# Kernel optimization log

Hardware: AMD Instinct MI355X
Metric: run time of the kernel (lower is better)

Reference implementation:

```python
import jax, jax.numpy as jnp
import numpy as np

G = 251            # grid_size = int(1e6 ** 0.4)
ORDER = 3          # KAN_SPLINE_ORDER
NB = G + ORDER     # num_basis = 254
H = (1.05 - (-0.05)) / G
# grid: [-order .. G+order] * h + lo  -> length G + 2*ORDER + 1 = 258 (same for every feature)
GRID = jnp.arange(-ORDER, G + ORDER + 1, dtype=jnp.float32) * H + (-0.05)
EPS = 1e-8


def bsplines(x):
    # x: [B, in] -> bases: [B, in, NB] via Cox-de Boor recursion
    x = x[..., None]
    b = ((x >= GRID[:-1]) & (x < GRID[1:])).astype(x.dtype)
    for k in range(1, ORDER + 1):
        left = (x - GRID[:-(k + 1)]) / jnp.maximum(GRID[k:-1] - GRID[:-(k + 1)], EPS)
        right = (GRID[k + 1:] - x) / jnp.maximum(GRID[k + 1:] - GRID[1:-k], EPS)
        b = left * b[..., :-1] + right * b[..., 1:]
    return b


def kan_layer(x, bw, sw, wb, ws, residual):
    # base path: SiLU then linear
    base = jax.nn.silu(x) @ bw.T                      # [B, out]
    # spline path: basis [B, in*NB] @ spline_weight.reshape(out, in*NB).T
    bas = bsplines(x).reshape(x.shape[0], -1)
    spl = bas @ sw.reshape(sw.shape[0], -1).T         # [B, out]
    out = wb * base + ws * spl
    return out + x if residual else out


def setup_inputs() -> dict:
    key = jax.random.key(0)
    ks = jax.random.split(key, 20)
    B, D, W = 2048, 64, 256
    d = {"x": jax.random.uniform(ks[0], (B, D), dtype=jnp.float32)}
    dims = [(W, D), (W, W), (W, W), (1, W)]
    for i, (o, inp) in enumerate(dims):
        d[f"bw{i}"] = jax.random.normal(ks[1 + 4 * i], (o, inp), dtype=jnp.float32) * 0.05
        d[f"sw{i}"] = jax.random.normal(ks[2 + 4 * i], (o, inp, NB), dtype=jnp.float32) * (0.5 / G)
        d[f"wb{i}"] = jnp.ones((1,), jnp.float32)
        d[f"ws{i}"] = jnp.ones((1,), jnp.float32)
    return d


def reference(x, bw0, sw0, wb0, ws0, bw1, sw1, wb1, ws1, bw2, sw2, wb2, ws2, bw3, sw3, wb3, ws3):
    h = kan_layer(x, bw0, sw0, wb0, ws0, False)   # input layer, no residual (64 -> 256)
    h = kan_layer(h, bw1, sw1, wb1, ws1, True)    # hidden, residual (256 -> 256)
    h = kan_layer(h, bw2, sw2, wb2, ws2, True)    # hidden, residual (256 -> 256)
    return kan_layer(h, bw3, sw3, wb3, ws3, False)  # output layer (256 -> 1)
```

## Files before the change

kernel.cpp:

```cpp
#include <hip/hip_runtime.h>

#define BATCH 2048
#define NB 254

typedef float f4u __attribute__((ext_vector_type(4), aligned(4)));

__device__ __forceinline__ float selw(int pd, float w0, float w1, float w2, float w3) {
    return (pd == 0) ? w0 : (pd == 1) ? w1 : (pd == 2) ? w2 : (pd == 3) ? w3 : 0.f;
}

template<bool TR>
__global__ __launch_bounds__(256) void basis_kernel(
    const float* __restrict__ act, int IN,
    const float* __restrict__ wbp, const float* __restrict__ wsp,
    float2* __restrict__ sjbuf, float4* __restrict__ vbuf)
{
    int idx = blockIdx.x * 256 + threadIdx.x;
    int total = BATCH * IN;
    if (idx >= total) return;
    int i = idx / BATCH;
    int b = idx - i * BATCH;

    float x = TR ? act[idx] : act[(size_t)b * IN + i];
    float wb = wbp[0], wsc = wsp[0];

    float sil = x / (1.f + __expf(-x));

    const float LO = -0.05f;
    const float INVH = 228.18181818181818f;
    float uf = (x - LO) * INVH;
    float fm = floorf(uf);
    float t = uf - fm;
    int M = (int)fm + 3;

    bool valid = (M >= 0) && (M <= 256);
    float wsv = valid ? wsc : 0.f;

    float omt = 1.f - t;
    float t2 = t * t, t3 = t2 * t;
    const float S = 1.f / 6.f;
    float w0 = omt * omt * omt * S * wsv;
    float w1 = (3.f * t3 - 6.f * t2 + 4.f) * S * wsv;
    float w2 = (-3.f * t3 + 3.f * t2 + 3.f * t + 1.f) * S * wsv;
    float w3 = t3 * S * wsv;

    int js = M - 3;
    js = js < 0 ? 0 : js;
    js = js > (NB - 4) ? (NB - 4) : js;
    if (!valid) js = 0;
    int d = js - (M - 3);

    float vp0 = selw(0 + d, w0, w1, w2, w3);
    float vp1 = selw(1 + d, w0, w1, w2, w3);
    float vp2 = selw(2 + d, w0, w1, w2, w3);
    float vp3 = selw(3 + d, w0, w1, w2, w3);

    sjbuf[idx] = make_float2(sil * wb, __int_as_float(js));
    vbuf[idx] = make_float4(vp0, vp1, vp2, vp3);
}

template<int IN, int OT, bool RES, int IG, int BT>
__global__ __launch_bounds__(BT * IG) void accum_f32(
    const float2* __restrict__ sjbuf, const float4* __restrict__ vbuf,
    const float* __restrict__ bw, const float* __restrict__ sw,
    const float* __restrict__ resid, float* __restrict__ out)
{
    int bx = threadIdx.x;
    int g  = threadIdx.y;
    int b  = blockIdx.y * BT + bx;
    int o0 = blockIdx.x * OT;

    float acc[OT];
#pragma unroll
    for (int k = 0; k < OT; k++) acc[k] = 0.f;

    const size_t ostride = (size_t)IN * NB;
    const int CH = IN / IG;
    const int i0 = g * CH;

    for (int ii = 0; ii < CH; ii++) {
        int i = i0 + ii;
        float2 sj = sjbuf[i * BATCH + b];
        float4 v = vbuf[i * BATCH + b];
        int j = __float_as_int(sj.y);
        float s = sj.x;
        const float* p = sw + (size_t)(o0 * IN + i) * NB + j;
        const float* bq = bw + (size_t)o0 * IN + i;

        f4u w[OT];
#pragma unroll
        for (int oo = 0; oo < OT; oo++)
            w[oo] = *(const f4u*)(p + (size_t)oo * ostride);

#pragma unroll
        for (int oo = 0; oo < OT; oo++) {
            float bwv = bq[oo * IN];
            acc[oo] += s * bwv + v.x * w[oo][0] + v.y * w[oo][1] + v.z * w[oo][2] + v.w * w[oo][3];
        }
    }

    __shared__ float lds[OT * (IG - 1) * BT];
    if (g > 0) {
#pragma unroll
        for (int oo = 0; oo < OT; oo++)
            lds[(oo * (IG - 1) + (g - 1)) * BT + bx] = acc[oo];
    }
    __syncthreads();
    if (g == 0) {
#pragma unroll
        for (int oo = 0; oo < OT; oo++) {
            float a = acc[oo];
            for (int gg = 1; gg < IG; gg++)
                a += lds[(oo * (IG - 1) + (gg - 1)) * BT + bx];
            size_t oidx = (size_t)(o0 + oo) * BATCH + b;
            float r = RES ? resid[oidx] : 0.f;
            out[oidx] = a + r;
        }
    }
}

__global__ __launch_bounds__(256) void out_kernel(
    const float2* __restrict__ sjbuf, const float4* __restrict__ vbuf,
    const float* __restrict__ bw, const float* __restrict__ sw,
    float* __restrict__ out)
{
    int tid = threadIdx.x;
    int bl = tid >> 6;
    int ig = tid & 63;
    int b = blockIdx.x * 4 + bl;

    float acc = 0.f;
    for (int ii = ig; ii < 256; ii += 64) {
        float2 sj = sjbuf[ii * BATCH + b];
        float4 v = vbuf[ii * BATCH + b];
        int j = __float_as_int(sj.y);
        const float* p = sw + (size_t)ii * NB + j;
        acc += sj.x * bw[ii] + v.x * p[0] + v.y * p[1] + v.z * p[2] + v.w * p[3];
    }
#pragma unroll
    for (int dlt = 32; dlt >= 1; dlt >>= 1) acc += __shfl_down(acc, dlt, 64);
    if (ig == 0) out[b] = acc;
}

extern "C" void kernel_launch(void* const* d_in, const int* in_sizes, int n_in,
                              void* d_out, int out_size, void* d_ws, size_t ws_size,
                              hipStream_t stream)
{
    const float* x   = (const float*)d_in[0];
    const float* bw0 = (const float*)d_in[1];
    const float* sw0 = (const float*)d_in[2];
    const float* wb0 = (const float*)d_in[3];
    const float* ws0 = (const float*)d_in[4];
    const float* bw1 = (const float*)d_in[5];
    const float* sw1 = (const float*)d_in[6];
    const float* wb1 = (const float*)d_in[7];
    const float* ws1 = (const float*)d_in[8];
    const float* bw2 = (const float*)d_in[9];
    const float* sw2 = (const float*)d_in[10];
    const float* wb2 = (const float*)d_in[11];
    const float* ws2 = (const float*)d_in[12];
    const float* bw3 = (const float*)d_in[13];
    const float* sw3 = (const float*)d_in[14];
    const float* wb3 = (const float*)d_in[15];
    const float* ws3 = (const float*)d_in[16];

    char* ws = (char*)d_ws;
    float4* vbuf  = (float4*)(ws);
    float2* sjbuf = (float2*)(ws + 8  * 1024 * 1024);
    float*  hA    = (float*)(ws + 12 * 1024 * 1024);
    float*  hB    = (float*)(ws + 14 * 1024 * 1024);

    float* out = (float*)d_out;

    dim3 ablk(64, 8);
    dim3 agrd(32, 32);

    basis_kernel<false><<<(BATCH * 64 + 255) / 256, 256, 0, stream>>>(x, 64, wb0, ws0, sjbuf, vbuf);
    accum_f32<64, 8, false, 8, 64><<<agrd, ablk, 0, stream>>>(sjbuf, vbuf, bw0, sw0, nullptr, hA);

    basis_kernel<true><<<(BATCH * 256 + 255) / 256, 256, 0, stream>>>(hA, 256, wb1, ws1, sjbuf, vbuf);
    accum_f32<256, 8, true, 8, 64><<<agrd, ablk, 0, stream>>>(sjbuf, vbuf, bw1, sw1, hA, hB);

    basis_kernel<true><<<(BATCH * 256 + 255) / 256, 256, 0, stream>>>(hB, 256, wb2, ws2, sjbuf, vbuf);
    accum_f32<256, 8, true, 8, 64><<<agrd, ablk, 0, stream>>>(sjbuf, vbuf, bw2, sw2, hB, hA);

    basis_kernel<true><<<(BATCH * 256 + 255) / 256, 256, 0, stream>>>(hA, 256, wb3, ws3, sjbuf, vbuf);
    out_kernel<<<BATCH / 4, 256, 0, stream>>>(sjbuf, vbuf, bw3, sw3, out);
}
```

Baseline: 295.2 us.

## Transpose spline weights to basis-major layout and use batch-major accumulation

```diff
diff --git a/kernel.cpp b/kernel.cpp
--- a/kernel.cpp
+++ b/kernel.cpp
@@ -9,7 +9,7 @@
     return (pd == 0) ? w0 : (pd == 1) ? w1 : (pd == 2) ? w2 : (pd == 3) ? w3 : 0.f;
 }
 
-template<bool TR>
+template<bool TR, bool BI>
 __global__ __launch_bounds__(256) void basis_kernel(
     const float* __restrict__ act, int IN,
     const float* __restrict__ wbp, const float* __restrict__ wsp,
@@ -18,10 +18,11 @@
     int idx = blockIdx.x * 256 + threadIdx.x;
     int total = BATCH * IN;
     if (idx >= total) return;
-    int i = idx / BATCH;
-    int b = idx - i * BATCH;
-
-    float x = TR ? act[idx] : act[(size_t)b * IN + i];
+    int i, b;
+    if (BI) { b = idx / IN; i = idx - b * IN; }
+    else    { i = idx / BATCH; b = idx - i * BATCH; }
+
+    float x = TR ? act[i * BATCH + b] : act[(size_t)b * IN + i];
     float wb = wbp[0], wsc = wsp[0];
 
     float sil = x / (1.f + __expf(-x));
@@ -57,6 +58,98 @@
 
     sjbuf[idx] = make_float2(sil * wb, __int_as_float(js));
     vbuf[idx] = make_float4(vp0, vp1, vp2, vp3);
+}
+
+__global__ __launch_bounds__(256) void transpose_sw(
+    const float* __restrict__ src, float* __restrict__ dst, int IN)
+{
+    __shared__ float lds[64][68];
+    int i  = blockIdx.z;
+    int c0 = blockIdx.y * 64;
+    int o0 = blockIdx.x * 64;
+    int t  = threadIdx.x;
+    int q16 = (t & 15) * 4;
+    int row = t >> 4;
+
+    for (int r = 0; r < 4; r++) {
+        int o = row + r * 16;
+        int c = c0 + q16;
+        const float* sp = src + ((size_t)(o0 + o) * IN + i) * NB + c;
+        if (c + 3 < NB) {
+            f4u v = *(const f4u*)sp;
+            lds[o][q16 + 0] = v[0]; lds[o][q16 + 1] = v[1];
+            lds[o][q16 + 2] = v[2]; lds[o][q16 + 3] = v[3];
+        } else {
+            for (int q = 0; q < 4; q++)
+                lds[o][q16 + q] = (c + q < NB) ? sp[q] : 0.f;
+        }
+    }
+    __syncthreads();
+    for (int r = 0; r < 4; r++) {
+        int cl = row + r * 16;
+        int c = c0 + cl;
+        if (c < NB) {
+            float4 v = make_float4(lds[q16 + 0][cl], lds[q16 + 1][cl],
+                                   lds[q16 + 2][cl], lds[q16 + 3][cl]);
+            *(float4*)(dst + ((size_t)i * NB + c) * 256 + o0 + q16) = v;
+        }
+    }
+}
+
+__global__ __launch_bounds__(256) void transpose_bw(
+    const float* __restrict__ src, float* __restrict__ dst, int IN, int O)
+{
+    __shared__ float lds[64][65];
+    int o0 = blockIdx.x * 64, i0 = blockIdx.y * 64;
+    int t = threadIdx.x; int tx = t & 63, ty = t >> 6;
+    for (int r = 0; r < 16; r++) {
+        int o = ty + r * 4;
+        lds[o][tx] = src[(size_t)(o0 + o) * IN + i0 + tx];
+    }
+    __syncthreads();
+    for (int r = 0; r < 16; r++) {
+        int irow = ty + r * 4;
+        dst[(size_t)(i0 + irow) * O + o0 + tx] = lds[tx][irow];
+    }
+}
+
+template<int IN, bool RES>
+__global__ __launch_bounds__(512) void accum_T(
+    const float2* __restrict__ sjbuf,
+    const float4* __restrict__ vbuf,
+    const float* __restrict__ swT,
+    const float* __restrict__ bwT,
+    const float* __restrict__ resid,
+    float* __restrict__ out)
+{
+    int lane = threadIdx.x;
+    int w    = threadIdx.y;
+    int b    = blockIdx.x * 8 + w;
+    int o0   = blockIdx.y * 128 + lane * 2;
+
+    const float2* sj = sjbuf + (size_t)b * IN;
+    const float4* vv = vbuf + (size_t)b * IN;
+
+    float a0 = 0.f, a1 = 0.f;
+
+#pragma unroll 4
+    for (int i = 0; i < IN; i++) {
+        float2 s = sj[i];
+        float4 v = vv[i];
+        int j = __float_as_int(s.y);
+        const float* tp = swT + ((size_t)i * NB + j) * 256 + o0;
+        float2 t0 = *(const float2*)(tp);
+        float2 t1 = *(const float2*)(tp + 256);
+        float2 t2 = *(const float2*)(tp + 512);
+        float2 t3 = *(const float2*)(tp + 768);
+        float2 bwv = *(const float2*)(bwT + (size_t)i * 256 + o0);
+        a0 += s.x * bwv.x + v.x * t0.x + v.y * t1.x + v.z * t2.x + v.w * t3.x;
+        a1 += s.x * bwv.y + v.x * t0.y + v.y * t1.y + v.z * t2.y + v.w * t3.y;
+    }
+    size_t oidx = (size_t)b * 256 + o0;
+    float r0 = 0.f, r1 = 0.f;
+    if (RES) { float2 rr = *(const float2*)(resid + oidx); r0 = rr.x; r1 = rr.y; }
+    *(float2*)(out + oidx) = make_float2(a0 + r0, a1 + r1);
 }
 
 template<int IN, int OT, bool RES, int IG, int BT>
@@ -86,16 +179,14 @@
         float s = sj.x;
         const float* p = sw + (size_t)(o0 * IN + i) * NB + j;
         const float* bq = bw + (size_t)o0 * IN + i;
-
-        f4u w[OT];
+        f4u wreg[OT];
 #pragma unroll
         for (int oo = 0; oo < OT; oo++)
-            w[oo] = *(const f4u*)(p + (size_t)oo * ostride);
-
+            wreg[oo] = *(const f4u*)(p + (size_t)oo * ostride);
 #pragma unroll
         for (int oo = 0; oo < OT; oo++) {
             float bwv = bq[oo * IN];
-            acc[oo] += s * bwv + v.x * w[oo][0] + v.y * w[oo][1] + v.z * w[oo][2] + v.w * w[oo][3];
+            acc[oo] += s * bwv + v.x * wreg[oo][0] + v.y * wreg[oo][1] + v.z * wreg[oo][2] + v.w * wreg[oo][3];
         }
     }
 
@@ -119,6 +210,7 @@
     }
 }
 
+template<bool BI>
 __global__ __launch_bounds__(256) void out_kernel(
     const float2* __restrict__ sjbuf, const float4* __restrict__ vbuf,
     const float* __restrict__ bw, const float* __restrict__ sw,
@@ -131,8 +223,9 @@
 
     float acc = 0.f;
     for (int ii = ig; ii < 256; ii += 64) {
-        float2 sj = sjbuf[ii * BATCH + b];
-        float4 v = vbuf[ii * BATCH + b];
+        int idx = BI ? (b * 256 + ii) : (ii * BATCH + b);
+        float2 sj = sjbuf[idx];
+        float4 v = vbuf[idx];
         int j = __float_as_int(sj.y);
         const float* p = sw + (size_t)ii * NB + j;
         acc += sj.x * bw[ii] + v.x * p[0] + v.y * p[1] + v.z * p[2] + v.w * p[3];
@@ -170,20 +263,61 @@
     float*  hA    = (float*)(ws + 12 * 1024 * 1024);
     float*  hB    = (float*)(ws + 14 * 1024 * 1024);
 
+    const size_t SWT0_OFF = 16777216u;
+    const size_t SWT0_SZ  = (size_t)64  * NB * 256 * 4;
+    const size_t SWT1_OFF = SWT0_OFF + SWT0_SZ;
+    const size_t SWT1_SZ  = (size_t)256 * NB * 256 * 4;
+    const size_t SWT2_OFF = SWT1_OFF + SWT1_SZ;
+    const size_t BWT0_OFF = SWT2_OFF + SWT1_SZ;
+    const size_t BWT1_OFF = BWT0_OFF + 65536u;
+    const size_t BWT2_OFF = BWT1_OFF + 262144u;
+    const size_t NEED     = BWT2_OFF + 262144u;
+
+    float* swT0 = (float*)(ws + SWT0_OFF);
+    float* swT1 = (float*)(ws + SWT1_OFF);
+    float* swT2 = (float*)(ws + SWT2_OFF);
+    float* bwT0 = (float*)(ws + BWT0_OFF);
+    float* bwT1 = (float*)(ws + BWT1_OFF);
+    float* bwT2 = (float*)(ws + BWT2_OFF);
+
     float* out = (float*)d_out;
-
-    dim3 ablk(64, 8);
-    dim3 agrd(32, 32);
-
-    basis_kernel<false><<<(BATCH * 64 + 255) / 256, 256, 0, stream>>>(x, 64, wb0, ws0, sjbuf, vbuf);
-    accum_f32<64, 8, false, 8, 64><<<agrd, ablk, 0, stream>>>(sjbuf, vbuf, bw0, sw0, nullptr, hA);
-
-    basis_kernel<true><<<(BATCH * 256 + 255) / 256, 256, 0, stream>>>(hA, 256, wb1, ws1, sjbuf, vbuf);
-    accum_f32<256, 8, true, 8, 64><<<agrd, ablk, 0, stream>>>(sjbuf, vbuf, bw1, sw1, hA, hB);
-
-    basis_kernel<true><<<(BATCH * 256 + 255) / 256, 256, 0, stream>>>(hB, 256, wb2, ws2, sjbuf, vbuf);
-    accum_f32<256, 8, true, 8, 64><<<agrd, ablk, 0, stream>>>(sjbuf, vbuf, bw2, sw2, hB, hA);
-
-    basis_kernel<true><<<(BATCH * 256 + 255) / 256, 256, 0, stream>>>(hA, 256, wb3, ws3, sjbuf, vbuf);
-    out_kernel<<<BATCH / 4, 256, 0, stream>>>(sjbuf, vbuf, bw3, sw3, out);
-}
+    bool fast = (ws_size >= NEED);
+
+    if (fast) {
+        transpose_sw<<<dim3(4, 4, 64),  256, 0, stream>>>(sw0, swT0, 64);
+        transpose_sw<<<dim3(4, 4, 256), 256, 0, stream>>>(sw1, swT1, 256);
+        transpose_sw<<<dim3(4, 4, 256), 256, 0, stream>>>(sw2, swT2, 256);
+        transpose_bw<<<dim3(4, 1), 256, 0, stream>>>(bw0, bwT0, 64, 256);
+        transpose_bw<<<dim3(4, 4), 256, 0, stream>>>(bw1, bwT1, 256, 256);
+        transpose_bw<<<dim3(4, 4), 256, 0, stream>>>(bw2, bwT2, 256, 256);
+
+        dim3 ablk(64, 8);
+        dim3 agrd(BATCH / 8, 2);
+
+        basis_kernel<false, true><<<BATCH * 64 / 256, 256, 0, stream>>>(x, 64, wb0, ws0, sjbuf, vbuf);
+        accum_T<64, false><<<agrd, ablk, 0, stream>>>(sjbuf, vbuf, swT0, bwT0, nullptr, hA);
+
+        basis_kernel<false, true><<<BATCH * 256 / 256, 256, 0, stream>>>(hA, 256, wb1, ws1, sjbuf, vbuf);
+        accum_T<256, true><<<agrd, ablk, 0, stream>>>(sjbuf, vbuf, swT1, bwT1, hA, hB);
+
+        basis_kernel<false, true><<<BATCH * 256 / 256, 256, 0, stream>>>(hB, 256, wb2, ws2, sjbuf, vbuf);
+        accum_T<256, true><<<agrd, ablk, 0, stream>>>(sjbuf, vbuf, swT2, bwT2, hB, hA);
+
+        basis_kernel<false, true><<<BATCH * 256 / 256, 256, 0, stream>>>(hA, 256, wb3, ws3, sjbuf, vbuf);
+        out_kernel<true><<<BATCH / 4, 256, 0, stream>>>(sjbuf, vbuf, bw3, sw3, out);
+    } else {
+        dim3 ablk(64, 8);
+        dim3 agrd(32, 32);
+        basis_kernel<false, false><<<BATCH * 64 / 256, 256, 0, stream>>>(x, 64, wb0, ws0, sjbuf, vbuf);
+        accum_f32<64, 8, false, 8, 64><<<agrd, ablk, 0, stream>>>(sjbuf, vbuf, bw0, sw0, nullptr, hA);
+
+        basis_kernel<true, false><<<BATCH * 256 / 256, 256, 0, stream>>>(hA, 256, wb1, ws1, sjbuf, vbuf);
+        accum_f32<256, 8, true, 8, 64><<<agrd, ablk, 0, stream>>>(sjbuf, vbuf, bw1, sw1, hA, hB);
+
+        basis_kernel<true, false><<<BATCH * 256 / 256, 256, 0, stream>>>(hB, 256, wb2, ws2, sjbuf, vbuf);
+        accum_f32<256, 8, true, 8, 64><<<agrd, ablk, 0, stream>>>(sjbuf, vbuf, bw2, sw2, hB, hA);
+
+        basis_kernel<true, false><<<BATCH * 256 / 256, 256, 0, stream>>>(hA, 256, wb3, ws3, sjbuf, vbuf);
+        out_kernel<false><<<BATCH / 4, 256, 0, stream>>>(sjbuf, vbuf, bw3, sw3, out);
+    }
+}
```

Result: slower. 561.8 us (+90.3%).
